# Kernel optimization log

Hardware: AMD Instinct MI355X
Metric: run time of the kernel (lower is better)

## Reference

```python
import jax, jax.numpy as jnp
import numpy as np

B, N, E, D, H = 128, 256, 1024, 128, 8
DK = D // H
NEG = -9e15

def _xavier(key, shape):
    lim = np.sqrt(6.0 / (shape[0] + shape[1]))
    return jax.random.uniform(key, shape, jnp.float32, -lim, lim)

def setup_inputs() -> dict:
    key = jax.random.key(0)
    ks = jax.random.split(key, 10)
    x = jax.random.normal(ks[0], (B, N, D), jnp.float32)
    mask = jax.random.randint(ks[1], (B, N), 0, 2) > 0
    mask = mask.at[:, 0].set(True)  # ensure no fully-masked molecule
    # unique (row, col) edges per molecule -> scatter .set matches torch index_put
    perm = jax.vmap(lambda k: jax.random.permutation(k, N * N)[:E])(jax.random.split(ks[2], B))
    edge_index = jnp.stack([perm // N, perm % N], axis=1).astype(jnp.int32)  # [B, 2, E]
    edge_attr = jax.random.normal(ks[3], (B, E, D), jnp.float32)
    return {
        "x": x, "mask": mask, "edge_index": edge_index, "edge_attr": edge_attr,
        "Wq": _xavier(ks[4], (D + 2, D)),
        "Wk": _xavier(ks[5], (D + 2, D)),
        "Wv": _xavier(ks[6], (D + 2, D)),
        "We_w": _xavier(ks[7], (D, D)),
        "We_b": jax.random.normal(ks[8], (D,), jnp.float32) * 0.02,
        "ln_g": jnp.ones((D,), jnp.float32),
        "ln_b": jnp.zeros((D,), jnp.float32),
    }

def reference(x, mask, edge_index, edge_attr, Wq, Wk, Wv, We_w, We_b, ln_g, ln_b):
    rows, cols = edge_index[:, 0, :], edge_index[:, 1, :]  # [B, E]
    # per-molecule degree features (torch_geometric.degree per row/col)
    deg = lambda idx: jax.vmap(lambda r: jnp.zeros((N,), x.dtype).at[r].add(1.0))(idx)
    deg_r, deg_c = deg(rows), deg(cols)
    x_new = jnp.concatenate([x, deg_r[..., None], deg_c[..., None]], axis=-1)  # [B,N,D+2]
    # edge bias: linear -> mean over features -> scatter into [B,N,N]
    edge_feats = (edge_attr @ We_w + We_b).mean(axis=-1)  # [B, E]
    edge_bias = jax.vmap(lambda r, c, f: jnp.zeros((N, N), x.dtype).at[r, c].set(f))(rows, cols, edge_feats)
    q = (x_new @ Wq).reshape(B, N, H, DK).transpose(0, 2, 1, 3)
    k = (x_new @ Wk).reshape(B, N, H, DK).transpose(0, 2, 1, 3)
    v = (x_new @ Wv).reshape(B, N, H, DK).transpose(0, 2, 1, 3)
    scores = jnp.einsum('bhqd,bhkd->bhqk', q, k) / np.sqrt(DK).astype(x.dtype)
    # mask keys first, then add edge bias (matches torch op order)
    scores = jnp.where(mask[:, None, None, :], scores, NEG) + edge_bias[:, None, :, :]
    attn = jax.nn.softmax(scores, axis=-1)  # dropout is identity in eval
    out = jnp.einsum('bhqk,bhkd->bhqd', attn, v).transpose(0, 2, 1, 3).reshape(B, N, D)
    out = out + x
    mu = out.mean(axis=-1, keepdims=True)
    var = out.var(axis=-1, keepdims=True)
    return (out - mu) / jnp.sqrt(var + 1e-6) * ln_g + ln_b
```

## Files before the change

### kernel.cpp

```cpp
#include <hip/hip_runtime.h>
#include <stdint.h>

#define NB 128
#define NN 256
#define NE 1024
#define ND 128
#define NH 8
#define NDK 16
#define NEGV -9.0e15f

typedef unsigned short u16;
typedef unsigned int u32;
typedef unsigned char u8;
typedef __attribute__((ext_vector_type(8))) short short8;
typedef __attribute__((ext_vector_type(4))) float float4v;

__device__ __forceinline__ float bf2f(u16 u) { return __uint_as_float(((u32)u) << 16); }
__device__ __forceinline__ u16 f2bf(float f) {
    u32 u = __float_as_uint(f);
    u += 0x7fffu + ((u >> 16) & 1u);
    return (u16)(u >> 16);
}
__device__ __forceinline__ float ldf(const void* p, size_t i, int f32) {
    return f32 ? ((const float*)p)[i] : bf2f(((const u16*)p)[i]);
}
__device__ __forceinline__ void stf(void* p, size_t i, int f32, float v) {
    if (f32) ((float*)p)[i] = v;
    else ((u16*)p)[i] = f2bf(v);
}
__device__ __forceinline__ void unpack8(uint4 a, float* o) {
    o[0] = bf2f(a.x & 0xffff); o[1] = bf2f(a.x >> 16);
    o[2] = bf2f(a.y & 0xffff); o[3] = bf2f(a.y >> 16);
    o[4] = bf2f(a.z & 0xffff); o[5] = bf2f(a.z >> 16);
    o[6] = bf2f(a.w & 0xffff); o[7] = bf2f(a.w >> 16);
}
union Pack8 { u16 u[8]; u32 w[4]; short8 v; };

__global__ __launch_bounds__(256) void k_init(const u16* x16, const u8* m8,
                                              const void* Wew, const void* Web,
                                              int* flags, float* wmean) {
    __shared__ u32 sev[256], sg1[256], smx[256];
    __shared__ int f32sh;
    int tid = threadIdx.x;
    u32 ev = 0;
    for (int i = tid * 128; i < tid * 128 + 128; ++i) {
        u32 e = (x16[i] >> 7) & 0xffu;
        ev |= (e >= 0xC2u) ? 1u : 0u;
    }
    u32 g1 = 0, mx = 0;
    for (int i = 0; i < 128; ++i) {
        u32 bv = m8[tid * 128 + i];
        if ((i & 3) == 1) g1 |= bv;
        mx = mx > bv ? mx : bv;
    }
    sev[tid] = ev; sg1[tid] = g1; smx[tid] = mx;
    __syncthreads();
    for (int s = 128; s > 0; s >>= 1) {
        if (tid < s) {
            sev[tid] |= sev[tid + s];
            sg1[tid] |= sg1[tid + s];
            smx[tid] = smx[tid] > smx[tid + s] ? smx[tid] : smx[tid + s];
        }
        __syncthreads();
    }
    if (tid == 0) {
        flags[0] = sev[0] ? 1 : 0;
        flags[1] = (sg1[0] == 0) ? 4 : ((smx[0] <= 1u) ? 1 : 2);
        f32sh = flags[0];
    }
    __syncthreads();
    int f32 = f32sh;
    if (tid < 128) {
        float s = 0.f;
        for (int d = 0; d < ND; ++d) s += ldf(Wew, (size_t)tid * ND + d, f32);
        wmean[tid] = s * (1.0f / ND);
    } else if (tid == 128) {
        float bsum = 0.f;
        for (int d = 0; d < ND; ++d) bsum += ldf(Web, d, f32);
        wmean[ND] = bsum * (1.0f / ND);
    }
}

__global__ __launch_bounds__(256) void k_efeat(const void* ea, const float* wmean,
                                               const int* flags, float* featsE) {
    __shared__ __align__(16) float swm[132];
    int tid = threadIdx.x;
    int f32 = flags[0];
    if (tid <= ND) swm[tid] = wmean[tid];
    __syncthreads();
    int sub = tid & 15, grp = tid >> 4;
    size_t eidx = (size_t)blockIdx.x * 16 + grp;
    const float4* wv = (const float4*)&swm[sub * 8];
    float4 w0 = wv[0], w1 = wv[1];
    size_t base = eidx * ND + sub * 8;
    float part;
    if (f32) {
        const float4* p = (const float4*)((const float*)ea + base);
        float4 a0 = p[0], a1 = p[1];
        part = a0.x * w0.x + a0.y * w0.y + a0.z * w0.z + a0.w * w0.w +
               a1.x * w1.x + a1.y * w1.y + a1.z * w1.z + a1.w * w1.w;
    } else {
        uint4 a = *(const uint4*)((const u16*)ea + base);
        float xv[8];
        unpack8(a, xv);
        part = xv[0] * w0.x + xv[1] * w0.y + xv[2] * w0.z + xv[3] * w0.w +
               xv[4] * w1.x + xv[5] * w1.y + xv[6] * w1.z + xv[7] * w1.w;
    }
    part += __shfl_xor(part, 1);
    part += __shfl_xor(part, 2);
    part += __shfl_xor(part, 4);
    part += __shfl_xor(part, 8);
    if (sub == 0) featsE[eidx] = part + swm[ND];
}

__global__ __launch_bounds__(256) void k_csr(const int* ei, const float* featsE,
                                             float* degr, float* degc,
                                             int* tstartG, u32* recsG) {
    __shared__ int cr[NN], cc[NN], tcnt[256], toffs[256], ts[257];
    int b = blockIdx.x, tid = threadIdx.x;
    cr[tid] = 0; cc[tid] = 0; tcnt[tid] = 0;
    __syncthreads();
    const int* rows = ei + (size_t)b * 2 * NE;
    const int* cols = rows + NE;
    for (int e = tid; e < NE; e += 256) {
        int r = rows[e], c = cols[e];
        atomicAdd(&cr[r], 1);
        atomicAdd(&cc[c], 1);
        atomicAdd(&tcnt[((c >> 4) << 4) | (r >> 4)], 1);
    }
    __syncthreads();
    degr[b * NN + tid] = (float)cr[tid];
    degc[b * NN + tid] = (float)cc[tid];
    if (tid == 0) {
        int a = 0;
        for (int t = 0; t < 256; ++t) { ts[t] = a; a += tcnt[t]; }
        ts[256] = a;
    }
    __syncthreads();
    toffs[tid] = ts[tid];
    tstartG[b * 257 + tid] = ts[tid];
    if (tid == 0) tstartG[b * 257 + 256] = ts[256];
    __syncthreads();
    for (int e = tid; e < NE; e += 256) {
        int r = rows[e], c = cols[e];
        float f = featsE[(size_t)b * NE + e];
        int t = ((c >> 4) << 4) | (r >> 4);
        int pos = atomicAdd(&toffs[t], 1);
        u32 rec = ((u32)f2bf(f) << 16) | ((u32)(c & 3) << 6) |
                  (u32)((r & 15) | (((c >> 2) & 3) << 4));
        recsG[(size_t)b * NE + pos] = rec;
    }
}

__global__ __launch_bounds__(64) void k_packB(const void* Wq, const void* Wk,
                                              const void* Wv, const int* flags, u16* WP) {
    int kT = blockIdx.x / 24, nT = blockIdx.x % 24;
    int lane = threadIdx.x;
    int col = lane & 15, quad = lane >> 4;
    int n = nT * 16 + col;
    int mat = n >> 7, nm = n & 127;
    const void* W = (mat == 0) ? Wq : (mat == 1) ? Wk : Wv;
    int f32 = flags[0];
    Pack8 c;
#pragma unroll
    for (int j = 0; j < 8; ++j) {
        int k = kT * 32 + quad * 8 + j;
        c.u[j] = (k < 130) ? f2bf(ldf(W, (size_t)k * ND + nm, f32)) : (u16)0;
    }
    *(short8*)(WP + ((size_t)(kT * 24 + nT) * 64 + lane) * 8) = c.v;
}

__global__ __launch_bounds__(256) void k_gemm(const void* x, const float* degr,
                                              const float* degc, const u16* WP,
                                              const int* flags, u16* qw, u16* kw, u16* vt) {
    int tid = threadIdx.x;
    int w = tid >> 6, lane = tid & 63;
    int quad = lane >> 4, col = lane & 15;
    int m0 = blockIdx.x * 64 + w * 16;
    int row = m0 + col;
    int f32 = flags[0];

    float4v acc[24];
#pragma unroll
    for (int t = 0; t < 24; ++t) acc[t] = (float4v){0.f, 0.f, 0.f, 0.f};

    const short8* wp = (const short8*)WP;
    for (int kT = 0; kT < 5; ++kT) {
        short8 a;
        if (kT < 4) {
            if (!f32) {
                a = *(const short8*)((const u16*)x + (size_t)row * ND + kT * 32 + quad * 8);
            } else {
                const float* xf = (const float*)x + (size_t)row * ND + kT * 32 + quad * 8;
                Pack8 c;
#pragma unroll
                for (int j = 0; j < 8; ++j) c.u[j] = f2bf(xf[j]);
                a = c.v;
            }
        } else {
            Pack8 c;
#pragma unroll
            for (int j = 0; j < 8; ++j) c.u[j] = 0;
            if (quad == 0) {
                c.u[0] = f2bf(degr[row]);
                c.u[1] = f2bf(degc[row]);
            }
            a = c.v;
        }
#pragma unroll
        for (int nT = 0; nT < 24; ++nT) {
            short8 bfr = wp[(size_t)(kT * 24 + nT) * 64 + lane];
            acc[nT] = __builtin_amdgcn_mfma_f32_16x16x32_bf16(a, bfr, acc[nT], 0, 0, 0);
        }
    }
    int bb = m0 >> 8;
    int nodebase = (m0 & 255) + quad * 4;
#pragma unroll
    for (int nT = 0; nT < 16; ++nT) {
        int h = nT & 7;
        u16* O = (nT < 8) ? qw : kw;
        size_t base = ((size_t)bb * NH + h) * NN + nodebase;
#pragma unroll
        for (int reg = 0; reg < 4; ++reg)
            O[(base + reg) * NDK + col] = f2bf(acc[nT][reg]);
    }
#pragma unroll
    for (int nT = 16; nT < 24; ++nT) {
        int h = nT - 16;
        u32 lo = (u32)f2bf(acc[nT][0]) | ((u32)f2bf(acc[nT][1]) << 16);
        u32 hi = (u32)f2bf(acc[nT][2]) | ((u32)f2bf(acc[nT][3]) << 16);
        uint2 pk = make_uint2(lo, hi);
        *(uint2*)(vt + (((size_t)bb * NH + h) * NDK + col) * NN + nodebase) = pk;
    }
}

__global__ __launch_bounds__(256) void k_attn(const u16* qg, const u16* kg,
                                              const u16* vt, const void* mask,
                                              const int* flags, const int* tstartG,
                                              const u32* recsG, void* out) {
    __shared__ __align__(16) u16 Ks[NN][24];
    __shared__ __align__(16) u16 Vs[NDK][264];
    __shared__ __align__(16) float mb[NN];
    __shared__ u32 recsS[NE];
    __shared__ int tstartS[257];
    __shared__ float lbuf[NN];
    int h = blockIdx.x, b = blockIdx.y, tid = threadIdx.x;
    int wv = tid >> 6, lane = tid & 63;
    int col = lane & 15, g = lane >> 4;
    int f32 = flags[0], mw = flags[1];
    size_t hb = ((size_t)b * NH + h) * NN;
    {
        const uint4* src = (const uint4*)(kg + (hb + tid) * NDK);
        uint4 a0 = src[0], a1 = src[1];
        uint4* dst = (uint4*)&Ks[tid][0];
        dst[0] = a0; dst[1] = a1;
    }
    {
        int dk = tid >> 4, chunk = tid & 15;
        const uint4* src = (const uint4*)(vt + ((size_t)(b * NH + h) * NDK + dk) * NN + chunk * 16);
        uint4 a0 = src[0], a1 = src[1];
        uint4* dst = (uint4*)&Vs[dk][chunk * 16];
        dst[0] = a0; dst[1] = a1;
    }
    {
        size_t mi = (size_t)b * NN + tid;
        bool mv;
        if (mw == 4)      mv = ((const u32*)mask)[mi] != 0;
        else if (mw == 2) mv = ((const u16*)mask)[mi] != 0;
        else              mv = ((const u8*)mask)[mi] != 0;
        mb[tid] = mv ? 0.0f : NEGV;
    }
    for (int e = tid; e < NE; e += 256) recsS[e] = recsG[(size_t)b * NE + e];
    tstartS[tid] = tstartG[b * 257 + tid];
    if (tid == 0) tstartS[256] = tstartG[b * 257 + 256];
    short8 qf[4];
#pragma unroll
    for (int qt = 0; qt < 4; ++qt) {
        int qtabs = wv * 4 + qt;
        short8 qv = {0, 0, 0, 0, 0, 0, 0, 0};
        if (g < 2)
            qv = *(const short8*)(qg + (hb + qtabs * 16 + col) * NDK + 8 * g);
        qf[qt] = qv;
    }
    __syncthreads();

    float4v outv[4];
    float lpart[4];
#pragma unroll
    for (int qt = 0; qt < 4; ++qt) {
        outv[qt] = (float4v){0.f, 0.f, 0.f, 0.f};
        lpart[qt] = 0.f;
    }

    for (int kt = 0; kt < 16; ++kt) {
        short8 kf = {0, 0, 0, 0, 0, 0, 0, 0};
        if (g < 2) kf = *(const short8*)&Ks[kt * 16 + col][8 * g];
        Pack8 vv;
        {
            uint2 t2 = *(const uint2*)&Vs[col][kt * 16 + 4 * g];
            vv.w[0] = t2.x; vv.w[1] = t2.y; vv.w[2] = 0; vv.w[3] = 0;
        }
        float4 mb4 = *(const float4*)&mb[kt * 16 + 4 * g];
#pragma unroll
        for (int qt = 0; qt < 4; ++qt) {
            float4v s4 = __builtin_amdgcn_mfma_f32_16x16x32_bf16(
                kf, qf[qt], (float4v){0.f, 0.f, 0.f, 0.f}, 0, 0, 0);
            float s0 = s4[0] * 0.25f + mb4.x;
            float s1 = s4[1] * 0.25f + mb4.y;
            float s2 = s4[2] * 0.25f + mb4.z;
            float s3 = s4[3] * 0.25f + mb4.w;
            int t = kt * 16 + wv * 4 + qt;
            int e1 = tstartS[t + 1];
            for (int e = tstartS[t]; e < e1; ++e) {
                u32 rec = recsS[e];
                float fb = bf2f((u16)(rec >> 16));
                bool lh = (lane == (int)(rec & 63u));
                int rg = (rec >> 6) & 3;
                s0 += (lh && rg == 0) ? fb : 0.f;
                s1 += (lh && rg == 1) ? fb : 0.f;
                s2 += (lh && rg == 2) ? fb : 0.f;
                s3 += (lh && rg == 3) ? fb : 0.f;
            }
            float p0 = __expf(fminf(s0, 60.f));
            float p1 = __expf(fminf(s1, 60.f));
            float p2 = __expf(fminf(s2, 60.f));
            float p3 = __expf(fminf(s3, 60.f));
            lpart[qt] += (p0 + p1) + (p2 + p3);
            Pack8 pp;
            pp.w[0] = (u32)f2bf(p0) | ((u32)f2bf(p1) << 16);
            pp.w[1] = (u32)f2bf(p2) | ((u32)f2bf(p3) << 16);
            pp.w[2] = 0; pp.w[3] = 0;
            outv[qt] = __builtin_amdgcn_mfma_f32_16x16x32_bf16(pp.v, vv.v, outv[qt], 0, 0, 0);
        }
    }
#pragma unroll
    for (int qt = 0; qt < 4; ++qt) {
        float l = lpart[qt];
        l += __shfl_xor(l, 16);
        l += __shfl_xor(l, 32);
        if (g == 0) lbuf[(wv * 4 + qt) * 16 + col] = l;
    }
    __syncthreads();
#pragma unroll
    for (int qt = 0; qt < 4; ++qt) {
        int qtabs = wv * 4 + qt;
#pragma unroll
        for (int reg = 0; reg < 4; ++reg) {
            int q = qtabs * 16 + 4 * g + reg;
            float val = outv[qt][reg] * (1.0f / lbuf[q]);
            stf(out, ((size_t)(b * NN + q)) * ND + h * NDK + col, f32, val);
        }
    }
}

__global__ __launch_bounds__(256) void k_ln(void* out, const void* x, const void* g,
                                            const void* be, const int* flags) {
    int f32 = flags[0];
    int tid = threadIdx.x, wv = tid >> 6, lane = tid & 63;
    int row = blockIdx.x * 4 + wv;
    size_t base = (size_t)row * ND;
    float v0 = ldf(out, base + lane, f32) + ldf(x, base + lane, f32);
    float v1 = ldf(out, base + lane + 64, f32) + ldf(x, base + lane + 64, f32);
    float s = v0 + v1, ss = v0 * v0 + v1 * v1;
#pragma unroll
    for (int off = 32; off; off >>= 1) {
        s += __shfl_xor(s, off, 64);
        ss += __shfl_xor(ss, off, 64);
    }
    float mu = s * (1.0f / ND);
    float var = ss * (1.0f / ND) - mu * mu;
    float rs = rsqrtf(var + 1e-6f);
    float o0 = (v0 - mu) * rs * ldf(g, lane, f32) + ldf(be, lane, f32);
    float o1 = (v1 - mu) * rs * ldf(g, lane + 64, f32) + ldf(be, lane + 64, f32);
    stf(out, base + lane, f32, o0);
    stf(out, base + lane + 64, f32, o1);
}

extern "C" void kernel_launch(void* const* d_in, const int* in_sizes, int n_in,
                              void* d_out, int out_size, void* d_ws, size_t ws_size,
                              hipStream_t stream) {
    const void* x = d_in[0];
    const void* mask = d_in[1];
    const int* ei = (const int*)d_in[2];
    const void* ea = d_in[3];
    const void* Wq = d_in[4];
    const void* Wk = d_in[5];
    const void* Wv = d_in[6];
    const void* Wew = d_in[7];
    const void* Web = d_in[8];
    const void* lng = d_in[9];
    const void* lnb = d_in[10];

    char* ws = (char*)d_ws;
    size_t off = 0;
    int* flags = (int*)(ws + off);       off += 256;
    float* wmean = (float*)(ws + off);   off += 1024;
    float* degr = (float*)(ws + off);    off += (size_t)NB * NN * 4;
    float* degc = (float*)(ws + off);    off += (size_t)NB * NN * 4;
    int* tstart = (int*)(ws + off);      off += (size_t)NB * 257 * 4 + 512;
    u32* recs = (u32*)(ws + off);        off += (size_t)NB * NE * 4;
    float* featsE = (float*)(ws + off);  off += (size_t)NB * NE * 4;
    u16* WP = (u16*)(ws + off);          off += (size_t)5 * 24 * 64 * 8 * 2;
    const size_t qkv_elems = (size_t)NB * NH * NN * NDK;
    u16* qw = (u16*)(ws + off);          off += qkv_elems * 2;
    u16* kw = (u16*)(ws + off);          off += qkv_elems * 2;
    u16* vt = (u16*)(ws + off);          off += qkv_elems * 2;

    k_init<<<1, 256, 0, stream>>>((const u16*)x, (const u8*)mask, Wew, Web, flags, wmean);
    k_efeat<<<(NB * NE) / 16, 256, 0, stream>>>(ea, wmean, flags, featsE);
    k_csr<<<NB, 256, 0, stream>>>(ei, featsE, degr, degc, tstart, recs);
    k_packB<<<120, 64, 0, stream>>>(Wq, Wk, Wv, flags, WP);
    k_gemm<<<(NB * NN) / 64, 256, 0, stream>>>(x, degr, degc, WP, flags, qw, kw, vt);
    k_attn<<<dim3(NH, NB), 256, 0, stream>>>(qw, kw, vt, mask, flags, tstart, recs, d_out);
    k_ln<<<(NB * NN) / 4, 256, 0, stream>>>(d_out, x, lng, lnb, flags);
}
```

Baseline: 248.9 us.

## Apply sparse edge bias as post-hoc softmax correction instead of per-tile record scan

```diff
diff --git a/kernel.cpp b/kernel.cpp
--- a/kernel.cpp
+++ b/kernel.cpp
@@ -14,6 +14,7 @@
 typedef unsigned char u8;
 typedef __attribute__((ext_vector_type(8))) short short8;
 typedef __attribute__((ext_vector_type(4))) float float4v;
+typedef __attribute__((ext_vector_type(2))) float f32x2;
 
 __device__ __forceinline__ float bf2f(u16 u) { return __uint_as_float(((u32)u) << 16); }
 __device__ __forceinline__ u16 f2bf(float f) {
@@ -34,13 +35,17 @@
     o[4] = bf2f(a.z & 0xffff); o[5] = bf2f(a.z >> 16);
     o[6] = bf2f(a.w & 0xffff); o[7] = bf2f(a.w >> 16);
 }
+__device__ __forceinline__ f32x2 bfpair(u32 w) {
+    return (f32x2){__uint_as_float(w << 16), __uint_as_float(w & 0xffff0000u)};
+}
+__device__ __forceinline__ u32 pk_bf(float a, float b) {
+    return ((__float_as_uint(a) + 0x8000u) >> 16) |
+           ((__float_as_uint(b) + 0x8000u) & 0xffff0000u);
+}
 union Pack8 { u16 u[8]; u32 w[4]; short8 v; };
 
-__global__ __launch_bounds__(256) void k_init(const u16* x16, const u8* m8,
-                                              const void* Wew, const void* Web,
-                                              int* flags, float* wmean) {
+__global__ __launch_bounds__(256) void k_detect(const u16* x16, const u8* m8, int* flags) {
     __shared__ u32 sev[256], sg1[256], smx[256];
-    __shared__ int f32sh;
     int tid = threadIdx.x;
     u32 ev = 0;
     for (int i = tid * 128; i < tid * 128 + 128; ++i) {
@@ -48,9 +53,10 @@
         ev |= (e >= 0xC2u) ? 1u : 0u;
     }
     u32 g1 = 0, mx = 0;
-    for (int i = 0; i < 128; ++i) {
-        u32 bv = m8[tid * 128 + i];
-        if ((i & 3) == 1) g1 |= bv;
+    for (int i = 0; i < 16; ++i) {
+        int idx = tid * 16 + i;
+        u32 bv = m8[idx];
+        if ((idx & 3) == 1) g1 |= bv;
         mx = mx > bv ? mx : bv;
     }
     sev[tid] = ev; sg1[tid] = g1; smx[tid] = mx;
@@ -66,19 +72,19 @@
     if (tid == 0) {
         flags[0] = sev[0] ? 1 : 0;
         flags[1] = (sg1[0] == 0) ? 4 : ((smx[0] <= 1u) ? 1 : 2);
-        f32sh = flags[0];
-    }
-    __syncthreads();
-    int f32 = f32sh;
-    if (tid < 128) {
-        float s = 0.f;
-        for (int d = 0; d < ND; ++d) s += ldf(Wew, (size_t)tid * ND + d, f32);
-        wmean[tid] = s * (1.0f / ND);
-    } else if (tid == 128) {
-        float bsum = 0.f;
-        for (int d = 0; d < ND; ++d) bsum += ldf(Web, d, f32);
-        wmean[ND] = bsum * (1.0f / ND);
-    }
+    }
+}
+
+__global__ __launch_bounds__(64) void k_wmean(const void* Wew, const void* Web,
+                                              const int* flags, float* wmean) {
+    int k = blockIdx.x, lane = threadIdx.x;
+    int f32 = flags[0];
+    const void* src = (k < 128) ? Wew : Web;
+    size_t base = (k < 128) ? (size_t)k * ND : 0;
+    float s = ldf(src, base + lane, f32) + ldf(src, base + lane + 64, f32);
+#pragma unroll
+    for (int off = 32; off; off >>= 1) s += __shfl_xor(s, off, 64);
+    if (lane == 0) wmean[k] = s * (1.0f / ND);
 }
 
 __global__ __launch_bounds__(256) void k_efeat(const void* ea, const float* wmean,
@@ -114,41 +120,36 @@
 }
 
 __global__ __launch_bounds__(256) void k_csr(const int* ei, const float* featsE,
-                                             float* degr, float* degc,
-                                             int* tstartG, u32* recsG) {
-    __shared__ int cr[NN], cc[NN], tcnt[256], toffs[256], ts[257];
+                                             float* degr, float* degc, int* rowstartG,
+                                             u16* colsG, float* featsG) {
+    __shared__ int cr[NN], cc[NN], offs[NN], rs[NN + 1];
     int b = blockIdx.x, tid = threadIdx.x;
-    cr[tid] = 0; cc[tid] = 0; tcnt[tid] = 0;
+    cr[tid] = 0; cc[tid] = 0;
     __syncthreads();
     const int* rows = ei + (size_t)b * 2 * NE;
     const int* cols = rows + NE;
     for (int e = tid; e < NE; e += 256) {
-        int r = rows[e], c = cols[e];
-        atomicAdd(&cr[r], 1);
-        atomicAdd(&cc[c], 1);
-        atomicAdd(&tcnt[((c >> 4) << 4) | (r >> 4)], 1);
+        atomicAdd(&cr[rows[e]], 1);
+        atomicAdd(&cc[cols[e]], 1);
     }
     __syncthreads();
     degr[b * NN + tid] = (float)cr[tid];
     degc[b * NN + tid] = (float)cc[tid];
     if (tid == 0) {
         int a = 0;
-        for (int t = 0; t < 256; ++t) { ts[t] = a; a += tcnt[t]; }
-        ts[256] = a;
-    }
-    __syncthreads();
-    toffs[tid] = ts[tid];
-    tstartG[b * 257 + tid] = ts[tid];
-    if (tid == 0) tstartG[b * 257 + 256] = ts[256];
+        for (int n = 0; n < NN; ++n) { rs[n] = a; a += cr[n]; }
+        rs[NN] = a;
+    }
+    __syncthreads();
+    offs[tid] = rs[tid];
+    rowstartG[b * (NN + 1) + tid] = rs[tid];
+    if (tid == 0) rowstartG[b * (NN + 1) + NN] = rs[NN];
     __syncthreads();
     for (int e = tid; e < NE; e += 256) {
-        int r = rows[e], c = cols[e];
-        float f = featsE[(size_t)b * NE + e];
-        int t = ((c >> 4) << 4) | (r >> 4);
-        int pos = atomicAdd(&toffs[t], 1);
-        u32 rec = ((u32)f2bf(f) << 16) | ((u32)(c & 3) << 6) |
-                  (u32)((r & 15) | (((c >> 2) & 3) << 4));
-        recsG[(size_t)b * NE + pos] = rec;
+        int r = rows[e];
+        int pos = atomicAdd(&offs[r], 1);
+        colsG[(size_t)b * NE + pos] = (u16)cols[e];
+        featsG[(size_t)b * NE + pos] = featsE[(size_t)b * NE + e];
     }
 }
 
@@ -172,7 +173,8 @@
 
 __global__ __launch_bounds__(256) void k_gemm(const void* x, const float* degr,
                                               const float* degc, const u16* WP,
-                                              const int* flags, u16* qw, u16* kw, u16* vt) {
+                                              const int* flags, u16* qw, u16* kw,
+                                              u16* vw, u16* vt) {
     int tid = threadIdx.x;
     int w = tid >> 6, lane = tid & 63;
     int quad = lane >> 4, col = lane & 15;
@@ -219,31 +221,37 @@
     for (int nT = 0; nT < 16; ++nT) {
         int h = nT & 7;
         u16* O = (nT < 8) ? qw : kw;
+        float sc = (nT < 8) ? 0.25f : 1.0f;
         size_t base = ((size_t)bb * NH + h) * NN + nodebase;
 #pragma unroll
         for (int reg = 0; reg < 4; ++reg)
-            O[(base + reg) * NDK + col] = f2bf(acc[nT][reg]);
+            O[(base + reg) * NDK + col] = f2bf(acc[nT][reg] * sc);
     }
 #pragma unroll
     for (int nT = 16; nT < 24; ++nT) {
         int h = nT - 16;
+        size_t base = ((size_t)bb * NH + h) * NN + nodebase;
+#pragma unroll
+        for (int reg = 0; reg < 4; ++reg)
+            vw[(base + reg) * NDK + col] = f2bf(acc[nT][reg]);
         u32 lo = (u32)f2bf(acc[nT][0]) | ((u32)f2bf(acc[nT][1]) << 16);
         u32 hi = (u32)f2bf(acc[nT][2]) | ((u32)f2bf(acc[nT][3]) << 16);
-        uint2 pk = make_uint2(lo, hi);
-        *(uint2*)(vt + (((size_t)bb * NH + h) * NDK + col) * NN + nodebase) = pk;
+        *(uint2*)(vt + (((size_t)bb * NH + h) * NDK + col) * NN + nodebase) = make_uint2(lo, hi);
     }
 }
 
 __global__ __launch_bounds__(256) void k_attn(const u16* qg, const u16* kg,
-                                              const u16* vt, const void* mask,
-                                              const int* flags, const int* tstartG,
-                                              const u32* recsG, void* out) {
+                                              const u16* vw, const u16* vt,
+                                              const void* mask, const int* flags,
+                                              const int* rowstartG, const u16* colsG,
+                                              const float* featsG, void* out) {
     __shared__ __align__(16) u16 Ks[NN][24];
     __shared__ __align__(16) u16 Vs[NDK][264];
     __shared__ __align__(16) float mb[NN];
-    __shared__ u32 recsS[NE];
-    __shared__ int tstartS[257];
+    __shared__ __align__(16) float Of[NN * NDK];
     __shared__ float lbuf[NN];
+    __shared__ u16 colsS[NE];
+    __shared__ float featsS[NE];
     int h = blockIdx.x, b = blockIdx.y, tid = threadIdx.x;
     int wv = tid >> 6, lane = tid & 63;
     int col = lane & 15, g = lane >> 4;
@@ -270,9 +278,10 @@
         else              mv = ((const u8*)mask)[mi] != 0;
         mb[tid] = mv ? 0.0f : NEGV;
     }
-    for (int e = tid; e < NE; e += 256) recsS[e] = recsG[(size_t)b * NE + e];
-    tstartS[tid] = tstartG[b * 257 + tid];
-    if (tid == 0) tstartS[256] = tstartG[b * 257 + 256];
+    for (int e = tid; e < NE; e += 256) {
+        colsS[e] = colsG[(size_t)b * NE + e];
+        featsS[e] = featsG[(size_t)b * NE + e];
+    }
     short8 qf[4];
 #pragma unroll
     for (int qt = 0; qt < 4; ++qt) {
@@ -301,34 +310,18 @@
             vv.w[0] = t2.x; vv.w[1] = t2.y; vv.w[2] = 0; vv.w[3] = 0;
         }
         float4 mb4 = *(const float4*)&mb[kt * 16 + 4 * g];
+        float4v cin = (float4v){mb4.x, mb4.y, mb4.z, mb4.w};
 #pragma unroll
         for (int qt = 0; qt < 4; ++qt) {
-            float4v s4 = __builtin_amdgcn_mfma_f32_16x16x32_bf16(
-                kf, qf[qt], (float4v){0.f, 0.f, 0.f, 0.f}, 0, 0, 0);
-            float s0 = s4[0] * 0.25f + mb4.x;
-            float s1 = s4[1] * 0.25f + mb4.y;
-            float s2 = s4[2] * 0.25f + mb4.z;
-            float s3 = s4[3] * 0.25f + mb4.w;
-            int t = kt * 16 + wv * 4 + qt;
-            int e1 = tstartS[t + 1];
-            for (int e = tstartS[t]; e < e1; ++e) {
-                u32 rec = recsS[e];
-                float fb = bf2f((u16)(rec >> 16));
-                bool lh = (lane == (int)(rec & 63u));
-                int rg = (rec >> 6) & 3;
-                s0 += (lh && rg == 0) ? fb : 0.f;
-                s1 += (lh && rg == 1) ? fb : 0.f;
-                s2 += (lh && rg == 2) ? fb : 0.f;
-                s3 += (lh && rg == 3) ? fb : 0.f;
-            }
-            float p0 = __expf(fminf(s0, 60.f));
-            float p1 = __expf(fminf(s1, 60.f));
-            float p2 = __expf(fminf(s2, 60.f));
-            float p3 = __expf(fminf(s3, 60.f));
+            float4v s4 = __builtin_amdgcn_mfma_f32_16x16x32_bf16(kf, qf[qt], cin, 0, 0, 0);
+            float p0 = __expf(fminf(s4[0], 60.f));
+            float p1 = __expf(fminf(s4[1], 60.f));
+            float p2 = __expf(fminf(s4[2], 60.f));
+            float p3 = __expf(fminf(s4[3], 60.f));
             lpart[qt] += (p0 + p1) + (p2 + p3);
             Pack8 pp;
-            pp.w[0] = (u32)f2bf(p0) | ((u32)f2bf(p1) << 16);
-            pp.w[1] = (u32)f2bf(p2) | ((u32)f2bf(p3) << 16);
+            pp.w[0] = pk_bf(p0, p1);
+            pp.w[1] = pk_bf(p2, p3);
             pp.w[2] = 0; pp.w[3] = 0;
             outv[qt] = __builtin_amdgcn_mfma_f32_16x16x32_bf16(pp.v, vv.v, outv[qt], 0, 0, 0);
         }
@@ -339,18 +332,52 @@
         l += __shfl_xor(l, 16);
         l += __shfl_xor(l, 32);
         if (g == 0) lbuf[(wv * 4 + qt) * 16 + col] = l;
-    }
-    __syncthreads();
-#pragma unroll
-    for (int qt = 0; qt < 4; ++qt) {
-        int qtabs = wv * 4 + qt;
-#pragma unroll
-        for (int reg = 0; reg < 4; ++reg) {
-            int q = qtabs * 16 + 4 * g + reg;
-            float val = outv[qt][reg] * (1.0f / lbuf[q]);
-            stf(out, ((size_t)(b * NN + q)) * ND + h * NDK + col, f32, val);
-        }
-    }
+        int q0 = (wv * 4 + qt) * 16 + 4 * g;
+#pragma unroll
+        for (int reg = 0; reg < 4; ++reg)
+            Of[(q0 + reg) * NDK + col] = outv[qt][reg];
+    }
+    __syncthreads();
+
+    float lfin = lbuf[tid];
+    float* ofrow = &Of[tid * NDK];
+    {
+        const uint4* qp = (const uint4*)(qg + (hb + tid) * NDK);
+        uint4 qa_ = qp[0], qb_ = qp[1];
+        f32x2 qr[8];
+        qr[0] = bfpair(qa_.x); qr[1] = bfpair(qa_.y);
+        qr[2] = bfpair(qa_.z); qr[3] = bfpair(qa_.w);
+        qr[4] = bfpair(qb_.x); qr[5] = bfpair(qb_.y);
+        qr[6] = bfpair(qb_.z); qr[7] = bfpair(qb_.w);
+        int e0 = rowstartG[b * (NN + 1) + tid];
+        int e1 = rowstartG[b * (NN + 1) + tid + 1];
+        for (int e = e0; e < e1; ++e) {
+            int c = colsS[e];
+            float f = featsS[e];
+            const u32* kcw = (const u32*)&Ks[c][0];
+            f32x2 s2 = qr[0] * bfpair(kcw[0]);
+            s2 += qr[1] * bfpair(kcw[1]); s2 += qr[2] * bfpair(kcw[2]);
+            s2 += qr[3] * bfpair(kcw[3]); s2 += qr[4] * bfpair(kcw[4]);
+            s2 += qr[5] * bfpair(kcw[5]); s2 += qr[6] * bfpair(kcw[6]);
+            s2 += qr[7] * bfpair(kcw[7]);
+            float s = s2.x + s2.y + mb[c];
+            float dl = __expf(fminf(s + f, 60.f)) - __expf(fminf(s, 60.f));
+            lfin += dl;
+            const uint4* vp = (const uint4*)(vw + (hb + c) * NDK);
+            uint4 v0 = vp[0], v1 = vp[1];
+            f32x2 d2 = (f32x2){dl, dl};
+            f32x2* orow2 = (f32x2*)ofrow;
+            orow2[0] += d2 * bfpair(v0.x); orow2[1] += d2 * bfpair(v0.y);
+            orow2[2] += d2 * bfpair(v0.z); orow2[3] += d2 * bfpair(v0.w);
+            orow2[4] += d2 * bfpair(v1.x); orow2[5] += d2 * bfpair(v1.y);
+            orow2[6] += d2 * bfpair(v1.z); orow2[7] += d2 * bfpair(v1.w);
+        }
+    }
+    float inv = 1.0f / lfin;
+    size_t obase = ((size_t)(b * NN + tid)) * ND + h * NDK;
+#pragma unroll
+    for (int i = 0; i < NDK; ++i)
+        stf(out, obase + i, f32, ofrow[i] * inv);
 }
 
 __global__ __launch_bounds__(256) void k_ln(void* out, const void* x, const void* g,
@@ -397,20 +424,24 @@
     float* wmean = (float*)(ws + off);   off += 1024;
     float* degr = (float*)(ws + off);    off += (size_t)NB * NN * 4;
     float* degc = (float*)(ws + off);    off += (size_t)NB * NN * 4;
-    int* tstart = (int*)(ws + off);      off += (size_t)NB * 257 * 4 + 512;
-    u32* recs = (u32*)(ws + off);        off += (size_t)NB * NE * 4;
+    int* rowstart = (int*)(ws + off);    off += (size_t)NB * (NN + 1) * 4 + 512;
+    u16* colsG = (u16*)(ws + off);       off += (size_t)NB * NE * 2;
+    float* featsG = (float*)(ws + off);  off += (size_t)NB * NE * 4;
     float* featsE = (float*)(ws + off);  off += (size_t)NB * NE * 4;
     u16* WP = (u16*)(ws + off);          off += (size_t)5 * 24 * 64 * 8 * 2;
     const size_t qkv_elems = (size_t)NB * NH * NN * NDK;
     u16* qw = (u16*)(ws + off);          off += qkv_elems * 2;
     u16* kw = (u16*)(ws + off);          off += qkv_elems * 2;
+    u16* vw = (u16*)(ws + off);          off += qkv_elems * 2;
     u16* vt = (u16*)(ws + off);          off += qkv_elems * 2;
 
-    k_init<<<1, 256, 0, stream>>>((const u16*)x, (const u8*)mask, Wew, Web, flags, wmean);
+    k_detect<<<1, 256, 0, stream>>>((const u16*)x, (const u8*)mask, flags);
+    k_wmean<<<129, 64, 0, stream>>>(Wew, Web, flags, wmean);
     k_efeat<<<(NB * NE) / 16, 256, 0, stream>>>(ea, wmean, flags, featsE);
-    k_csr<<<NB, 256, 0, stream>>>(ei, featsE, degr, degc, tstart, recs);
+    k_csr<<<NB, 256, 0, stream>>>(ei, featsE, degr, degc, rowstart, colsG, featsG);
     k_packB<<<120, 64, 0, stream>>>(Wq, Wk, Wv, flags, WP);
-    k_gemm<<<(NB * NN) / 64, 256, 0, stream>>>(x, degr, degc, WP, flags, qw, kw, vt);
-    k_attn<<<dim3(NH, NB), 256, 0, stream>>>(qw, kw, vt, mask, flags, tstart, recs, d_out);
+    k_gemm<<<(NB * NN) / 64, 256, 0, stream>>>(x, degr, degc, WP, flags, qw, kw, vw, vt);
+    k_attn<<<dim3(NH, NB), 256, 0, stream>>>(qw, kw, vw, vt, mask, flags, rowstart,
+                                             colsG, featsG, d_out);
     k_ln<<<(NB * NN) / 4, 256, 0, stream>>>(d_out, x, lng, lnb, flags);
 }
```

Result: faster. 217.6 us (-12.6%).
